# Kernel optimization log

Hardware: AMD Instinct MI355X
Metric: run time of the kernel (lower is better)

The kernel has to match this reference:

```python
import math
import jax, jax.numpy as jnp
import numpy as np

# gpt-oss config constants (layer_idx=1 -> sliding_window disabled)
HID = 2880
N_HEADS = 64
N_KV = 8
D_HEAD = 64
GROUPS = N_HEADS // N_KV  # 8 query heads per kv head
SLIDING_WINDOW = 0        # layer_idx % 2 == 1 -> full causal attention
SM_SCALE = 1.0 / math.sqrt(D_HEAD)
EPS = 1e-5

ROPE_BASE = 150000.0
INIT_CTX = 4096
SCALING = 32.0
NTK_ALPHA = 1.0
NTK_BETA = 32.0


def _rope_cos_sin(num_tokens: int):
    """YaRN-scaled RoPE tables, fp32, positions 0..num_tokens-1 (offset=0, no cache)."""
    d_half = D_HEAD // 2
    freq = ROPE_BASE ** (np.arange(0, D_HEAD, 2, dtype=np.float64) / D_HEAD)
    concentration = 0.1 * math.log(SCALING) + 1.0
    low = d_half * math.log(INIT_CTX / (NTK_BETA * 2 * math.pi)) / math.log(ROPE_BASE)
    high = d_half * math.log(INIT_CTX / (NTK_ALPHA * 2 * math.pi)) / math.log(ROPE_BASE)
    interpolation = 1.0 / (SCALING * freq)
    extrapolation = 1.0 / freq
    ramp = (np.arange(d_half, dtype=np.float64) - low) / (high - low)
    mask = 1.0 - np.clip(ramp, 0.0, 1.0)
    inv_freq = interpolation * (1.0 - mask) + extrapolation * mask
    t = np.arange(num_tokens, dtype=np.float64)
    freqs = np.outer(t, inv_freq)  # [S, d_half]
    cos = (np.cos(freqs) * concentration).astype(np.float32)
    sin = (np.sin(freqs) * concentration).astype(np.float32)
    return jnp.asarray(cos), jnp.asarray(sin)


def _rotate(x, cos, sin):
    # x: [B, S, nh, D]; cos/sin: [S, D/2]
    c = cos[None, :, None, :]
    s = sin[None, :, None, :]
    x1, x2 = jnp.split(x, 2, axis=-1)
    return jnp.concatenate([x1 * c - x2 * s, x2 * c + x1 * s], axis=-1)


def setup_inputs() -> dict:
    key = jax.random.key(0)
    ks = jax.random.split(key, 5)
    B, S = 1, 1536
    x = jax.random.normal(ks[0], (B, S, HID), dtype=jnp.float32)
    sinks = jax.random.normal(ks[1], (N_HEADS,), dtype=jnp.float32) * 0.5
    norm_scale = jnp.ones((HID,), dtype=jnp.float32)
    qkv_dim = D_HEAD * (N_HEADS + 2 * N_KV)  # 5120
    qkv_w = jax.random.normal(ks[2], (qkv_dim, HID), dtype=jnp.float32) * 0.02
    qkv_b = jnp.zeros((qkv_dim,), dtype=jnp.float32)
    out_w = jax.random.normal(ks[3], (HID, N_HEADS * D_HEAD), dtype=jnp.float32) * 0.02
    out_b = jnp.zeros((HID,), dtype=jnp.float32)
    return {"x": x, "sinks": sinks, "norm_scale": norm_scale,
            "qkv_w": qkv_w, "qkv_b": qkv_b, "out_w": out_w, "out_b": out_b}


def reference(x, sinks, norm_scale, qkv_w, qkv_b, out_w, out_b):
    B, S, _ = x.shape
    # RMSNorm (fp32)
    t = x * jax.lax.rsqrt(jnp.mean(x * x, axis=-1, keepdims=True) + EPS) * norm_scale
    # fused QKV projection
    qkv = jnp.einsum('bsd,od->bso', t, qkv_w) + qkv_b
    q, k, v = jnp.split(qkv, [N_HEADS * D_HEAD, (N_HEADS + N_KV) * D_HEAD], axis=-1)
    q = q.reshape(B, S, N_HEADS, D_HEAD)
    k = k.reshape(B, S, N_KV, D_HEAD)
    v = v.reshape(B, S, N_KV, D_HEAD)
    # RoPE (offset = 0, no cache)
    cos, sin = _rope_cos_sin(S)
    q = _rotate(q, cos, sin)
    k = _rotate(k, cos, sin)
    # GQA: head h = g*N_KV + kv
    q = q.reshape(B, S, GROUPS, N_KV, D_HEAD)
    scores = jnp.einsum('bqgkd,bskd->bgkqs', q, k) * SM_SCALE  # [B,G,KV,S,S]
    i = jnp.arange(S)[:, None]
    j = jnp.arange(S)[None, :]
    allowed = j <= i  # causal
    if SLIDING_WINDOW > 0:
        allowed = allowed & (i - j < SLIDING_WINDOW)
    scores = jnp.where(allowed[None, None, None, :, :], scores, -1e30)
    # softmax with learned per-head sink logit in the denominator
    sink = sinks.reshape(GROUPS, N_KV)[None, :, :, None]  # [1,G,KV,1]
    m = jnp.maximum(jnp.max(scores, axis=-1), sink)       # [B,G,KV,S]
    p = jnp.exp(scores - m[..., None])
    denom = jnp.sum(p, axis=-1) + jnp.exp(sink - m)
    attn = p / denom[..., None]
    o = jnp.einsum('bgkqs,bskd->bqgkd', attn, v).reshape(B, S, N_HEADS * D_HEAD)
    y = jnp.einsum('bse,oe->bso', o, out_w) + out_b
    return x + y
```

## Files before the change

### kernel.cpp

```cpp
#include <hip/hip_runtime.h>
#include <hip/hip_bf16.h>
#include <math.h>

typedef unsigned short u16;
typedef __attribute__((ext_vector_type(8))) short bf16x8;
typedef __attribute__((ext_vector_type(4))) float f32x4;
typedef __attribute__((ext_vector_type(4))) u16 u16x4;
typedef __attribute__((ext_vector_type(8))) u16 u16x8;

#define S_LEN   1536
#define HID     2880
#define NH      64
#define NKV     8
#define DH      64
#define QKV_N   5120
#define QDIM    4096
#define KVDIM   512
#define SMSCALE 0.125f
#define EPSV    1e-5f

__device__ __forceinline__ float b2f(u16 u) {
    unsigned int v = ((unsigned int)u) << 16;
    float f; __builtin_memcpy(&f, &v, 4); return f;
}
__device__ __forceinline__ u16 f2b(float f) {
    __hip_bfloat16 h = __float2bfloat16(f);
    return *reinterpret_cast<u16*>(&h);
}
__device__ __forceinline__ void gld16(const u16* g, u16* l) {
    __builtin_amdgcn_global_load_lds(
        (const __attribute__((address_space(1))) unsigned int*)g,
        (__attribute__((address_space(3))) unsigned int*)l, 16, 0, 0);
}
#define WAIT_VM6()   __builtin_amdgcn_s_waitcnt(0xF76)
#define WAIT_VM4()   __builtin_amdgcn_s_waitcnt(0xF74)
#define WAIT_VM0()   __builtin_amdgcn_s_waitcnt(0xF70)
#define WAIT_LGKM0() __builtin_amdgcn_s_waitcnt(0xC07F)

__global__ __launch_bounds__(256) void prep_kernel(
    const float* __restrict__ qkv_w, u16* __restrict__ qkv_w_bf,
    const float* __restrict__ x, const float* __restrict__ ns, u16* __restrict__ t,
    float* __restrict__ cosT, float* __restrict__ sinT,
    const float* __restrict__ out_w, u16* __restrict__ out_w_bf)
{
    __shared__ float red[4];
    const int b = blockIdx.x;
    const int tid = threadIdx.x;
    if (b < 14400) {
        int i = b * 256 + tid;
        float4 v = ((const float4*)qkv_w)[i];
        u16x4 o;
        o.x = f2b(v.x); o.y = f2b(v.y); o.z = f2b(v.z); o.w = f2b(v.w);
        ((u16x4*)qkv_w_bf)[i] = o;
    } else if (b < 15936) {
        const int s = b - 14400;
        const float* xr = x + (size_t)s * HID;
        float ss = 0.f;
        for (int i = tid; i < HID; i += 256) { float v = xr[i]; ss += v * v; }
        for (int off = 32; off > 0; off >>= 1) ss += __shfl_down(ss, off);
        if ((tid & 63) == 0) red[tid >> 6] = ss;
        __syncthreads();
        float tot = red[0] + red[1] + red[2] + red[3];
        float scale = rsqrtf(tot / (float)HID + EPSV);
        u16* tr = t + (size_t)s * HID;
        for (int i = tid; i < HID; i += 256)
            tr[i] = f2b(xr[i] * scale * ns[i]);
    } else if (b < 16128) {
        int idx = (b - 15936) * 256 + tid;
        if (idx >= S_LEN * 32) return;
        int s = idx >> 5, i = idx & 31;
        const double PI2 = 6.283185307179586476925286766559;
        double base = 150000.0;
        double freq = pow(base, (double)(2 * i) / 64.0);
        double conc = 0.1 * log(32.0) + 1.0;
        double low  = 32.0 * log(4096.0 / (32.0 * PI2)) / log(base);
        double high = 32.0 * log(4096.0 / (1.0  * PI2)) / log(base);
        double interp = 1.0 / (32.0 * freq);
        double extrap = 1.0 / freq;
        double ramp = ((double)i - low) / (high - low);
        double msk = 1.0 - fmin(fmax(ramp, 0.0), 1.0);
        double invf = interp * (1.0 - msk) + extrap * msk;
        double ang = (double)s * invf;
        cosT[idx] = (float)(cos(ang) * conc);
        sinT[idx] = (float)(sin(ang) * conc);
    } else {
        int i = (b - 16128) * 256 + tid;
        float4 v = ((const float4*)out_w)[i];
        u16x4 o;
        o.x = f2b(v.x); o.y = f2b(v.y); o.z = f2b(v.z); o.w = f2b(v.w);
        ((u16x4*)out_w_bf)[i] = o;
    }
}

__global__ __launch_bounds__(256) void conv_bf16_kernel(
    const float* __restrict__ src, u16* __restrict__ dst, int n4)
{
    int i = blockIdx.x * 256 + threadIdx.x;
    if (i >= n4) return;
    float4 v = ((const float4*)src)[i];
    u16x4 o;
    o.x = f2b(v.x); o.y = f2b(v.y); o.z = f2b(v.z); o.w = f2b(v.w);
    ((u16x4*)dst)[i] = o;
}

__global__ __launch_bounds__(512, 2) void gemm_bt_8p_kernel(
    const u16* __restrict__ A, const u16* __restrict__ B,
    u16* __restrict__ Cp, u16* __restrict__ Cp2, u16* __restrict__ Cp3,
    int M, int N, int K, int it0, int it1, int ntm, int ntn)
{
    extern __shared__ __align__(16) u16 smem[];
    u16* sAp = smem;
    u16* sBp = smem + 32768;

    const int tid  = threadIdx.x;
    const int wave = tid >> 6, lane = tid & 63;
    const int quad = lane >> 4, l16 = lane & 15;
    const int wm = wave >> 2, wn = wave & 3;

    const int nwg  = gridDim.x;
    const int q8   = nwg >> 3, r8 = nwg & 7;
    const int flat = blockIdx.x;
    const int xcd  = flat & 7, loc = flat >> 3;
    const int swz  = (xcd < r8) ? xcd * (q8 + 1) + loc
                                : r8 * (q8 + 1) + (xcd - r8) * q8 + loc;
    const int tpz  = ntm * ntn;
    const int z    = swz / tpz;
    const int rem  = swz - z * tpz;
    const int nt   = rem / ntm;
    const int mt   = rem - nt * ntm;
    const int bm = mt * 256, bn = nt * 256;
    const int niter = z ? it1 : it0;
    const int kb    = z ? (it0 + (z - 1) * it1) * 64 : 0;
    u16* C = (z == 0) ? Cp : (z == 1) ? (Cp + (size_t)M * N) : (z == 2) ? Cp2 : Cp3;

    const int r2  = tid >> 2;
    const int ks8 = (tid & 3) * 8;
    const u16* gA0 = A + (size_t)(bm + r2) * K + kb + ks8;
    const u16* gA1 = gA0 + (size_t)128 * K;
    int brA = bn + r2;       if (brA > N - 1) brA = N - 1;
    int brB = bn + 128 + r2; if (brB > N - 1) brB = N - 1;
    const u16* gB0 = B + (size_t)brA * K + kb + ks8;
    const u16* gB1 = B + (size_t)brB * K + kb + ks8;
    const int sw = wave * 512;

    f32x4 acc[8][4];
    #pragma unroll
    for (int i = 0; i < 8; i++)
        #pragma unroll
        for (int j = 0; j < 4; j++) acc[i][j] = (f32x4){0.f, 0.f, 0.f, 0.f};

    auto stA = [&](int c, int kh, int t) {
        u16* d = sAp + (((c << 1) | kh) << 13);
        const int koff = t * 64 + kh * 32;
        gld16(gA0 + koff, d + sw);
        gld16(gA1 + koff, d + 4096 + sw);
    };
    auto stB = [&](int c, int kh, int t) {
        u16* d = sBp + (((c << 1) | kh) << 13);
        const int koff = t * 64 + kh * 32;
        gld16(gB0 + koff, d + sw);
        gld16(gB1 + koff, d + 4096 + sw);
    };

    bf16x8 bv[4];
    const int arow = wm * 128 + l16;
    const int brow = wn * 64 + l16;
    auto rdB = [&](int c, int ks) {
        const u16* p = sBp + (((c << 1) | ks) << 13) + brow * 32 + quad * 8;
        #pragma unroll
        for (int nf = 0; nf < 4; nf++) bv[nf] = *(const bf16x8*)(p + nf * 16 * 32);
    };
    auto mmph = [&](int c, int ks, int mh) {
        const u16* p = sAp + (((c << 1) | ks) << 13) + (arow + mh * 64) * 32 + quad * 8;
        bf16x8 av[4];
        #pragma unroll
        for (int mf = 0; mf < 4; mf++) av[mf] = *(const bf16x8*)(p + mf * 16 * 32);
        __builtin_amdgcn_s_setprio(1);
        #pragma unroll
        for (int mf = 0; mf < 4; mf++)
            #pragma unroll
            for (int nf = 0; nf < 4; nf++)
                acc[mh * 4 + mf][nf] = __builtin_amdgcn_mfma_f32_16x16x32_bf16(
                    av[mf], bv[nf], acc[mh * 4 + mf][nf], 0, 0, 0);
        __builtin_amdgcn_s_setprio(0);
    };

    stA(0, 0, 0); stB(0, 0, 0); stA(0, 1, 0); stB(0, 1, 0);

    for (int t = 0; t < niter - 1; ++t) {
        const int c = t & 1;
        stA(c ^ 1, 0, t + 1);
        WAIT_VM6();
        __builtin_amdgcn_s_barrier();
        rdB(c, 0); mmph(c, 0, 0);
        stB(c ^ 1, 0, t + 1);
        mmph(c, 0, 1);
        stA(c ^ 1, 1, t + 1);
        WAIT_VM6();
        __builtin_amdgcn_s_barrier();
        rdB(c, 1); mmph(c, 1, 0);
        stB(c ^ 1, 1, t + 1);
        mmph(c, 1, 1);
    }
    {
        const int c = (niter - 1) & 1;
        WAIT_VM4();
        __builtin_amdgcn_s_barrier();
        rdB(c, 0); mmph(c, 0, 0); mmph(c, 0, 1);
        WAIT_VM0();
        __builtin_amdgcn_s_barrier();
        rdB(c, 1); mmph(c, 1, 0); mmph(c, 1, 1);
    }

    #pragma unroll
    for (int im = 0; im < 8; im++) {
        const int row0 = bm + wm * 128 + im * 16 + quad * 4;
        #pragma unroll
        for (int nf = 0; nf < 4; nf++) {
            const int col = bn + wn * 64 + nf * 16 + l16;
            if (col < N) {
                #pragma unroll
                for (int r = 0; r < 4; r++)
                    C[(size_t)(row0 + r) * N + col] = f2b(acc[im][nf][r]);
            }
        }
    }
}

__global__ __launch_bounds__(256) void rope_apply_kernel(
    const u16* __restrict__ p0, const u16* __restrict__ p1, const float* __restrict__ bias,
    const float* __restrict__ cosT, const float* __restrict__ sinT,
    u16* __restrict__ q_r, u16* __restrict__ k_r, u16* __restrict__ v_r)
{
    int idx = blockIdx.x * 256 + threadIdx.x;
    if (idx >= S_LEN * 320) return;
    int s = idx / 320;
    int c = idx - s * 320;
    const u16* r0p = p0 + (size_t)s * QKV_N;
    const u16* r1p = p1 + (size_t)s * QKV_N;
    if (c < 288) {
        int hh = c >> 2, j0 = (c & 3) * 8;
        int off = hh * 64;
        u16x8 a1 = *(const u16x8*)(r0p + off + j0);
        u16x8 b1 = *(const u16x8*)(r1p + off + j0);
        u16x8 a2 = *(const u16x8*)(r0p + off + 32 + j0);
        u16x8 b2 = *(const u16x8*)(r1p + off + 32 + j0);
        float bl[8], bh[8], cc[8], sn[8];
        *(float4*)&bl[0] = *(const float4*)(bias + off + j0);
        *(float4*)&bl[4] = *(const float4*)(bias + off + j0 + 4);
        *(float4*)&bh[0] = *(const float4*)(bias + off + 32 + j0);
        *(float4*)&bh[4] = *(const float4*)(bias + off + 32 + j0 + 4);
        *(float4*)&cc[0] = *(const float4*)(cosT + s * 32 + j0);
        *(float4*)&cc[4] = *(const float4*)(cosT + s * 32 + j0 + 4);
        *(float4*)&sn[0] = *(const float4*)(sinT + s * 32 + j0);
        *(float4*)&sn[4] = *(const float4*)(sinT + s * 32 + j0 + 4);
        const float scale = (hh < 64) ? SMSCALE : 1.0f;
        u16x8 lo, hi;
        #pragma unroll
        for (int j = 0; j < 8; j++) {
            float x1 = b2f(a1[j]) + b2f(b1[j]) + bl[j];
            float x2 = b2f(a2[j]) + b2f(b2[j]) + bh[j];
            lo[j] = f2b((x1 * cc[j] - x2 * sn[j]) * scale);
            hi[j] = f2b((x2 * cc[j] + x1 * sn[j]) * scale);
        }
        if (hh < 64) {
            u16* dst = q_r + (size_t)s * QDIM + off;
            *(u16x8*)(dst + j0) = lo;
            *(u16x8*)(dst + 32 + j0) = hi;
        } else {
            u16* dst = k_r + (size_t)s * KVDIM + (hh - 64) * 64;
            *(u16x8*)(dst + j0) = lo;
            *(u16x8*)(dst + 32 + j0) = hi;
        }
    } else {
        int c2 = c - 288;
        int vh = c2 >> 2, i0 = (c2 & 3) * 16;
        int off = QDIM + KVDIM + vh * 64 + i0;
        u16x8 a0 = *(const u16x8*)(r0p + off);
        u16x8 a1 = *(const u16x8*)(r0p + off + 8);
        u16x8 b0 = *(const u16x8*)(r1p + off);
        u16x8 b1 = *(const u16x8*)(r1p + off + 8);
        float bb[16];
        *(float4*)&bb[0]  = *(const float4*)(bias + off);
        *(float4*)&bb[4]  = *(const float4*)(bias + off + 4);
        *(float4*)&bb[8]  = *(const float4*)(bias + off + 8);
        *(float4*)&bb[12] = *(const float4*)(bias + off + 12);
        u16x8 o0, o1;
        #pragma unroll
        for (int j = 0; j < 8; j++) {
            o0[j] = f2b(b2f(a0[j]) + b2f(b0[j]) + bb[j]);
            o1[j] = f2b(b2f(a1[j]) + b2f(b1[j]) + bb[8 + j]);
        }
        u16* dst = v_r + (size_t)s * KVDIM + vh * 64 + i0;
        *(u16x8*)dst = o0;
        *(u16x8*)(dst + 8) = o1;
    }
}

__global__ __launch_bounds__(256) void vt_kernel(
    const u16* __restrict__ v_r, u16* __restrict__ vt)
{
    __shared__ u16 tile[64][72];
    const int s0 = blockIdx.x * 64;
    const int kvh = blockIdx.y;
    const int tid = threadIdx.x;
    const int r = tid >> 3;
    const int c = (tid & 7) * 8;

    #pragma unroll
    for (int rr = 0; rr < 64; rr += 32) {
        uint4 vv = *(const uint4*)(v_r + (size_t)(s0 + r + rr) * KVDIM + kvh * 64 + c);
        const u16* p = (const u16*)&vv;
        #pragma unroll
        for (int j = 0; j < 8; j++) tile[c + j][r + rr] = p[j];
    }
    __syncthreads();
    #pragma unroll
    for (int rr = 0; rr < 64; rr += 32) {
        uint4 ov;
        u16* p = (u16*)&ov;
        #pragma unroll
        for (int j = 0; j < 8; j++) p[j] = tile[r + rr][c + j];
        *(uint4*)(vt + (size_t)(kvh * 64 + r + rr) * S_LEN + s0 + c) = ov;
    }
}

__global__ __launch_bounds__(256) void attn_kernel(
    const u16* __restrict__ q_r, const u16* __restrict__ k_r, const u16* __restrict__ vt,
    const float* __restrict__ sinks, u16* __restrict__ o)
{
    __shared__ __align__(16) u16 sK[2][64 * 72];
    __shared__ __align__(16) u16 sVt[2][64 * 72];
    __shared__ __align__(16) u16 sP[4 * 16 * 72];

    const int bx = blockIdx.x, h = blockIdx.y;
    const int kvh = h & 7;
    const int tid = threadIdx.x, wave = tid >> 6, lane = tid & 63;
    const int quad = lane >> 4, l16 = lane & 15;
    const int srow = tid >> 3;
    const int scol = (tid & 7) * 8;
    u16* sPw = sP + wave * 16 * 72;
    const float sinkv = sinks[h];

    uint4 kreg0, kreg1, vreg0, vreg1;
    const u16* kbase = k_r + (size_t)srow * KVDIM + kvh * 64 + scol;
    const u16* vbase = vt + (size_t)(kvh * 64 + srow) * S_LEN + scol;

    auto issue = [&](int j0) {
        kreg0 = *(const uint4*)(kbase + (size_t)j0 * KVDIM);
        kreg1 = *(const uint4*)(kbase + (size_t)(j0 + 32) * KVDIM);
        vreg0 = *(const uint4*)(vbase + j0);
        vreg1 = *(const uint4*)(vbase + (size_t)32 * S_LEN + j0);
    };
    auto lwrite = [&](int c) {
        *(uint4*)(&sK[c][srow * 72 + scol])        = kreg0;
        *(uint4*)(&sK[c][(srow + 32) * 72 + scol]) = kreg1;
        *(uint4*)(&sVt[c][srow * 72 + scol])        = vreg0;
        *(uint4*)(&sVt[c][(srow + 32) * 72 + scol]) = vreg1;
    };

    for (int phase = 0; phase < 2; ++phase) {
        const int qt = phase ? (23 - bx) : bx;
        const int q_i = qt * 64 + wave * 16 + l16;
        const u16* qp = q_r + (size_t)q_i * QDIM + h * 64 + quad * 8;
        bf16x8 aq0 = *(const bf16x8*)(qp);
        bf16x8 aq1 = *(const bf16x8*)(qp + 32);

        float m_i = sinkv, l_i = 1.0f;
        f32x4 acc[4];
        #pragma unroll
        for (int dt = 0; dt < 4; dt++) acc[dt] = (f32x4){0.f, 0.f, 0.f, 0.f};

        const int ntile = qt + 1;
        issue(0);
        __syncthreads();

        for (int tt = 0; tt < ntile; ++tt) {
            const int c = tt & 1;
            lwrite(c);
            if (tt + 1 < ntile) issue((tt + 1) * 64);
            WAIT_LGKM0();
            __builtin_amdgcn_s_barrier();

            f32x4 sc[4];
            __builtin_amdgcn_s_setprio(1);
            #pragma unroll
            for (int nt = 0; nt < 4; nt++) {
                const u16* kp = &sK[c][(nt * 16 + l16) * 72 + quad * 8];
                bf16x8 bk0 = *(const bf16x8*)(kp);
                bf16x8 bk1 = *(const bf16x8*)(kp + 32);
                f32x4 s0 = (f32x4){0.f, 0.f, 0.f, 0.f};
                s0 = __builtin_amdgcn_mfma_f32_16x16x32_bf16(bk0, aq0, s0, 0, 0, 0);
                s0 = __builtin_amdgcn_mfma_f32_16x16x32_bf16(bk1, aq1, s0, 0, 0, 0);
                sc[nt] = s0;
            }
            __builtin_amdgcn_s_setprio(0);

            if (tt == qt) {
                #pragma unroll
                for (int nt = 0; nt < 4; nt++)
                    #pragma unroll
                    for (int r = 0; r < 4; r++)
                        if (tt * 64 + nt * 16 + quad * 4 + r > q_i) sc[nt][r] = -INFINITY;
            }

            float vmax = sc[0][0];
            #pragma unroll
            for (int nt = 0; nt < 4; nt++)
                #pragma unroll
                for (int r = 0; r < 4; r++) vmax = fmaxf(vmax, sc[nt][r]);
            vmax = fmaxf(vmax, __shfl_xor(vmax, 16));
            vmax = fmaxf(vmax, __shfl_xor(vmax, 32));
            if (__any(vmax > m_i + 8.0f)) {
                float mnew = fmaxf(m_i, vmax);
                float alpha = __expf(m_i - mnew);
                l_i *= alpha;
                #pragma unroll
                for (int dt = 0; dt < 4; dt++)
                    #pragma unroll
                    for (int r = 0; r < 4; r++) acc[dt][r] *= alpha;
                m_i = mnew;
            }
            float ps = 0.f;
            u16x4 pk[4];
            #pragma unroll
            for (int nt = 0; nt < 4; nt++) {
                #pragma unroll
                for (int r = 0; r < 4; r++) {
                    float p = __expf(sc[nt][r] - m_i);
                    ps += p;
                    pk[nt][r] = f2b(p);
                }
            }
            ps += __shfl_xor(ps, 16);
            ps += __shfl_xor(ps, 32);
            l_i += ps;
            #pragma unroll
            for (int nt = 0; nt < 4; nt++)
                *(u16x4*)(sPw + l16 * 72 + nt * 16 + quad * 4) = pk[nt];
            __threadfence_block();

            bf16x8 ap0 = *(const bf16x8*)(sPw + l16 * 72 + quad * 8);
            bf16x8 ap1 = *(const bf16x8*)(sPw + l16 * 72 + 32 + quad * 8);
            __builtin_amdgcn_s_setprio(1);
            #pragma unroll
            for (int dt = 0; dt < 4; dt++) {
                const u16* vp = &sVt[c][(dt * 16 + l16) * 72 + quad * 8];
                bf16x8 bv0 = *(const bf16x8*)(vp);
                bf16x8 bv1 = *(const bf16x8*)(vp + 32);
                acc[dt] = __builtin_amdgcn_mfma_f32_16x16x32_bf16(bv0, ap0, acc[dt], 0, 0, 0);
                acc[dt] = __builtin_amdgcn_mfma_f32_16x16x32_bf16(bv1, ap1, acc[dt], 0, 0, 0);
            }
            __builtin_amdgcn_s_setprio(0);
        }

        float inv = 1.0f / l_i;
        #pragma unroll
        for (int dt = 0; dt < 4; dt++) {
            u16x4 ov;
            #pragma unroll
            for (int r = 0; r < 4; r++) ov[r] = f2b(acc[dt][r] * inv);
            *(u16x4*)(o + (size_t)q_i * QDIM + h * 64 + dt * 16 + quad * 4) = ov;
        }
    }
}

__global__ __launch_bounds__(256) void final_add_kernel(
    const u16* __restrict__ p0, const u16* __restrict__ p1, const u16* __restrict__ p2,
    const u16* __restrict__ p3, int np,
    const float* __restrict__ bias, const float* __restrict__ x, float* __restrict__ out)
{
    int i = blockIdx.x * 256 + threadIdx.x;
    int base = i * 4;
    int col = base % HID;
    float4 xo = *(const float4*)(x + base);
    float4 bi = *(const float4*)(bias + col);
    u16x4 a = ((const u16x4*)p0)[i];
    u16x4 b = ((const u16x4*)p1)[i];
    u16x4 c = ((const u16x4*)p2)[i];
    float4 r;
    r.x = b2f(a.x) + b2f(b.x) + b2f(c.x) + bi.x + xo.x;
    r.y = b2f(a.y) + b2f(b.y) + b2f(c.y) + bi.y + xo.y;
    r.z = b2f(a.z) + b2f(b.z) + b2f(c.z) + bi.z + xo.z;
    r.w = b2f(a.w) + b2f(b.w) + b2f(c.w) + bi.w + xo.w;
    if (np == 4) {
        u16x4 d = ((const u16x4*)p3)[i];
        r.x += b2f(d.x); r.y += b2f(d.y); r.z += b2f(d.z); r.w += b2f(d.w);
    }
    *(float4*)(out + base) = r;
}

extern "C" void kernel_launch(void* const* d_in, const int* in_sizes, int n_in,
                              void* d_out, int out_size, void* d_ws, size_t ws_size,
                              hipStream_t stream)
{
    const float* x          = (const float*)d_in[0];
    const float* sinks      = (const float*)d_in[1];
    const float* norm_scale = (const float*)d_in[2];
    const float* qkv_w      = (const float*)d_in[3];
    const float* qkv_b      = (const float*)d_in[4];
    const float* out_w      = (const float*)d_in[5];
    const float* out_b      = (const float*)d_in[6];
    float* out = (float*)d_out;

    char* ws = (char*)d_ws;
    u16* t        = (u16*)(ws);
    u16* qkv_w_bf = (u16*)(ws + 8847360);
    u16* qkvp0    = (u16*)(ws + 38338560);
    u16* qkvp1    = (u16*)(ws + 54067200);
    float* cosT   = (float*)(ws + 69795840);
    float* sinT   = (float*)(ws + 69992448);
    u16* k_r      = (u16*)(ws);
    u16* vt       = (u16*)(ws + 1572864);
    u16* q_r      = (u16*)(ws + 3145728);
    u16* o        = (u16*)(ws + 15728640);
    u16* v_r      = (u16*)(ws + 28311552);
    u16* outp0    = (u16*)(ws + 28311552);
    u16* outp1    = (u16*)(ws + 37158912);
    u16* outp2    = (u16*)(ws + 3145728);

    const bool fuse_outw = (ws_size >= 93782016ull);
    u16* out_w_bf = fuse_outw ? (u16*)(ws + 70189056) : (u16*)(ws + 46006272);

    static bool lds_attr_set = false;
    if (!lds_attr_set) {
        hipFuncSetAttribute(reinterpret_cast<const void*>(gemm_bt_8p_kernel),
                            hipFuncAttributeMaxDynamicSharedMemorySize, 131072);
        lds_attr_set = true;
    }

    prep_kernel<<<fuse_outw ? 27648 : 16128, 256, 0, stream>>>(
        qkv_w, qkv_w_bf, x, norm_scale, t, cosT, sinT, out_w, out_w_bf);
    gemm_bt_8p_kernel<<<240, 512, 131072, stream>>>(
        t, qkv_w_bf, qkvp0, qkvp0, qkvp0, S_LEN, QKV_N, HID, 23, 22, 6, 20);
    rope_apply_kernel<<<(S_LEN * 320) / 256, 256, 0, stream>>>(
        qkvp0, qkvp1, qkv_b, cosT, sinT, q_r, k_r, v_r);
    vt_kernel<<<dim3(S_LEN / 64, NKV), 256, 0, stream>>>(v_r, vt);
    if (!fuse_outw)
        conv_bf16_kernel<<<(HID * QDIM / 4 + 255) / 256, 256, 0, stream>>>(out_w, out_w_bf, HID * QDIM / 4);
    attn_kernel<<<dim3(12, NH), 256, 0, stream>>>(q_r, k_r, vt, sinks, o);
    gemm_bt_8p_kernel<<<216, 512, 131072, stream>>>(
        o, out_w_bf, outp0, outp2, outp2, S_LEN, HID, QDIM, 22, 21, 6, 12);
    final_add_kernel<<<S_LEN * HID / 4 / 256, 256, 0, stream>>>(
        outp0, outp1, outp2, outp2, 3, out_b, x, out);
}
```

Before: 311.4 us.

## Fuse V transpose into RoPE kernel and switch softmax to exp2 domain

New measurement: 313.0 us. About the same (+0.5%).

```diff
diff --git a/kernel.cpp b/kernel.cpp
--- a/kernel.cpp
+++ b/kernel.cpp
@@ -17,6 +17,7 @@
 #define QDIM    4096
 #define KVDIM   512
 #define SMSCALE 0.125f
+#define LOG2E   1.44269504f
 #define EPSV    1e-5f
 
 __device__ __forceinline__ float b2f(u16 u) {
@@ -230,15 +231,17 @@
 __global__ __launch_bounds__(256) void rope_apply_kernel(
     const u16* __restrict__ p0, const u16* __restrict__ p1, const float* __restrict__ bias,
     const float* __restrict__ cosT, const float* __restrict__ sinT,
-    u16* __restrict__ q_r, u16* __restrict__ k_r, u16* __restrict__ v_r)
-{
-    int idx = blockIdx.x * 256 + threadIdx.x;
-    if (idx >= S_LEN * 320) return;
-    int s = idx / 320;
-    int c = idx - s * 320;
-    const u16* r0p = p0 + (size_t)s * QKV_N;
-    const u16* r1p = p1 + (size_t)s * QKV_N;
-    if (c < 288) {
+    u16* __restrict__ q_r, u16* __restrict__ k_r, u16* __restrict__ vt)
+{
+    __shared__ u16 tile[64][72];
+    const int b = blockIdx.x;
+    const int tid = threadIdx.x;
+    if (b < 1728) {
+        int idx = b * 256 + tid;
+        int s = idx / 288;
+        int c = idx - s * 288;
+        const u16* r0p = p0 + (size_t)s * QKV_N;
+        const u16* r1p = p1 + (size_t)s * QKV_N;
         int hh = c >> 2, j0 = (c & 3) * 8;
         int off = hh * 64;
         u16x8 a1 = *(const u16x8*)(r0p + off + j0);
@@ -254,7 +257,7 @@
         *(float4*)&cc[4] = *(const float4*)(cosT + s * 32 + j0 + 4);
         *(float4*)&sn[0] = *(const float4*)(sinT + s * 32 + j0);
         *(float4*)&sn[4] = *(const float4*)(sinT + s * 32 + j0 + 4);
-        const float scale = (hh < 64) ? SMSCALE : 1.0f;
+        const float scale = (hh < 64) ? SMSCALE * LOG2E : 1.0f;
         u16x8 lo, hi;
         #pragma unroll
         for (int j = 0; j < 8; j++) {
@@ -273,55 +276,33 @@
             *(u16x8*)(dst + 32 + j0) = hi;
         }
     } else {
-        int c2 = c - 288;
-        int vh = c2 >> 2, i0 = (c2 & 3) * 16;
-        int off = QDIM + KVDIM + vh * 64 + i0;
-        u16x8 a0 = *(const u16x8*)(r0p + off);
-        u16x8 a1 = *(const u16x8*)(r0p + off + 8);
-        u16x8 b0 = *(const u16x8*)(r1p + off);
-        u16x8 b1 = *(const u16x8*)(r1p + off + 8);
-        float bb[16];
-        *(float4*)&bb[0]  = *(const float4*)(bias + off);
-        *(float4*)&bb[4]  = *(const float4*)(bias + off + 4);
-        *(float4*)&bb[8]  = *(const float4*)(bias + off + 8);
-        *(float4*)&bb[12] = *(const float4*)(bias + off + 12);
-        u16x8 o0, o1;
-        #pragma unroll
-        for (int j = 0; j < 8; j++) {
-            o0[j] = f2b(b2f(a0[j]) + b2f(b0[j]) + bb[j]);
-            o1[j] = f2b(b2f(a1[j]) + b2f(b1[j]) + bb[8 + j]);
-        }
-        u16* dst = v_r + (size_t)s * KVDIM + vh * 64 + i0;
-        *(u16x8*)dst = o0;
-        *(u16x8*)(dst + 8) = o1;
-    }
-}
-
-__global__ __launch_bounds__(256) void vt_kernel(
-    const u16* __restrict__ v_r, u16* __restrict__ vt)
-{
-    __shared__ u16 tile[64][72];
-    const int s0 = blockIdx.x * 64;
-    const int kvh = blockIdx.y;
-    const int tid = threadIdx.x;
-    const int r = tid >> 3;
-    const int c = (tid & 7) * 8;
-
-    #pragma unroll
-    for (int rr = 0; rr < 64; rr += 32) {
-        uint4 vv = *(const uint4*)(v_r + (size_t)(s0 + r + rr) * KVDIM + kvh * 64 + c);
-        const u16* p = (const u16*)&vv;
-        #pragma unroll
-        for (int j = 0; j < 8; j++) tile[c + j][r + rr] = p[j];
-    }
-    __syncthreads();
-    #pragma unroll
-    for (int rr = 0; rr < 64; rr += 32) {
-        uint4 ov;
-        u16* p = (u16*)&ov;
-        #pragma unroll
-        for (int j = 0; j < 8; j++) p[j] = tile[r + rr][c + j];
-        *(uint4*)(vt + (size_t)(kvh * 64 + r + rr) * S_LEN + s0 + c) = ov;
+        int vb = b - 1728;
+        int kvh = vb / 24, sblk = vb - kvh * 24;
+        int s0 = sblk * 64;
+        int r = tid >> 3;
+        int cc = (tid & 7) * 8;
+        int off = QDIM + KVDIM + kvh * 64 + cc;
+        float bb[8];
+        *(float4*)&bb[0] = *(const float4*)(bias + off);
+        *(float4*)&bb[4] = *(const float4*)(bias + off + 4);
+        #pragma unroll
+        for (int rr = 0; rr < 64; rr += 32) {
+            int s = s0 + r + rr;
+            u16x8 a = *(const u16x8*)(p0 + (size_t)s * QKV_N + off);
+            u16x8 b2 = *(const u16x8*)(p1 + (size_t)s * QKV_N + off);
+            #pragma unroll
+            for (int j = 0; j < 8; j++)
+                tile[cc + j][r + rr] = f2b(b2f(a[j]) + b2f(b2[j]) + bb[j]);
+        }
+        __syncthreads();
+        #pragma unroll
+        for (int rr = 0; rr < 64; rr += 32) {
+            uint4 ov;
+            u16* p = (u16*)&ov;
+            #pragma unroll
+            for (int j = 0; j < 8; j++) p[j] = tile[r + rr][cc + j];
+            *(uint4*)(vt + (size_t)(kvh * 64 + r + rr) * S_LEN + s0 + cc) = ov;
+        }
     }
 }
 
@@ -340,7 +321,7 @@
     const int srow = tid >> 3;
     const int scol = (tid & 7) * 8;
     u16* sPw = sP + wave * 16 * 72;
-    const float sinkv = sinks[h];
+    const float sinkv = sinks[h] * LOG2E;
 
     uint4 kreg0, kreg1, vreg0, vreg1;
     const u16* kbase = k_r + (size_t)srow * KVDIM + kvh * 64 + scol;
@@ -411,9 +392,9 @@
                 for (int r = 0; r < 4; r++) vmax = fmaxf(vmax, sc[nt][r]);
             vmax = fmaxf(vmax, __shfl_xor(vmax, 16));
             vmax = fmaxf(vmax, __shfl_xor(vmax, 32));
-            if (__any(vmax > m_i + 8.0f)) {
+            if (__any(vmax > m_i + 11.0f)) {
                 float mnew = fmaxf(m_i, vmax);
-                float alpha = __expf(m_i - mnew);
+                float alpha = exp2f(m_i - mnew);
                 l_i *= alpha;
                 #pragma unroll
                 for (int dt = 0; dt < 4; dt++)
@@ -427,7 +408,7 @@
             for (int nt = 0; nt < 4; nt++) {
                 #pragma unroll
                 for (int r = 0; r < 4; r++) {
-                    float p = __expf(sc[nt][r] - m_i);
+                    float p = exp2f(sc[nt][r] - m_i);
                     ps += p;
                     pk[nt][r] = f2b(p);
                 }
@@ -514,7 +495,6 @@
     u16* vt       = (u16*)(ws + 1572864);
     u16* q_r      = (u16*)(ws + 3145728);
     u16* o        = (u16*)(ws + 15728640);
-    u16* v_r      = (u16*)(ws + 28311552);
     u16* outp0    = (u16*)(ws + 28311552);
     u16* outp1    = (u16*)(ws + 37158912);
     u16* outp2    = (u16*)(ws + 3145728);
@@ -533,9 +513,8 @@
         qkv_w, qkv_w_bf, x, norm_scale, t, cosT, sinT, out_w, out_w_bf);
     gemm_bt_8p_kernel<<<240, 512, 131072, stream>>>(
         t, qkv_w_bf, qkvp0, qkvp0, qkvp0, S_LEN, QKV_N, HID, 23, 22, 6, 20);
-    rope_apply_kernel<<<(S_LEN * 320) / 256, 256, 0, stream>>>(
-        qkvp0, qkvp1, qkv_b, cosT, sinT, q_r, k_r, v_r);
-    vt_kernel<<<dim3(S_LEN / 64, NKV), 256, 0, stream>>>(v_r, vt);
+    rope_apply_kernel<<<1920, 256, 0, stream>>>(
+        qkvp0, qkvp1, qkv_b, cosT, sinT, q_r, k_r, vt);
     if (!fuse_outw)
         conv_bf16_kernel<<<(HID * QDIM / 4 + 255) / 256, 256, 0, stream>>>(out_w, out_w_bf, HID * QDIM / 4);
     attn_kernel<<<dim3(12, NH), 256, 0, stream>>>(q_r, k_r, vt, sinks, o);
```
